# Kernel tuning notes

Measured on AMD Instinct MI355X. Metric: run time of the kernel, lower is better.

The kernel has to match this reference:

```python
import jax, jax.numpy as jnp
import numpy as np

N = 50000
E = 800000
IN_DIM = 256
HID = 256
OUT_DIM = 2


def setup_inputs() -> dict:
    key = jax.random.key(0)
    ks = jax.random.split(key, 10)
    x = jax.random.normal(ks[0], (N, IN_DIM), dtype=jnp.float32)
    edge_index = jax.random.randint(ks[1], (2, E), 0, N, dtype=jnp.int64)
    # Glorot-ish scaling so activations stay well-conditioned through 4 layers
    def w(k, fan_in, fan_out):
        return jax.random.normal(k, (fan_in, fan_out), dtype=jnp.float32) / jnp.sqrt(jnp.float32(fan_in))
    return {
        "x": x,
        "edge_index": edge_index,
        "W0": w(ks[2], IN_DIM, HID), "b0": jnp.zeros((HID,), jnp.float32),
        "W1": w(ks[3], HID, HID),    "b1": jnp.zeros((HID,), jnp.float32),
        "W2": w(ks[4], HID, HID),    "b2": jnp.zeros((HID,), jnp.float32),
        "W3": w(ks[5], HID, OUT_DIM), "b3": jnp.zeros((OUT_DIM,), jnp.float32),
    }


def _gcn_norm(edge_index, n, dtype):
    # PyG gcn_norm with self-loops: deg over destination, norm = d^-1/2[src]*d^-1/2[dst]
    loops = jnp.arange(n, dtype=edge_index.dtype)
    src = jnp.concatenate([edge_index[0], loops])
    dst = jnp.concatenate([edge_index[1], loops])
    deg = jax.ops.segment_sum(jnp.ones_like(dst, dtype=dtype), dst, num_segments=n)
    dis = deg ** -0.5  # deg >= 1 due to self-loops
    norm = dis[src] * dis[dst]
    return src, dst, norm


def reference(x, edge_index, W0, b0, W1, b1, W2, b2, W3, b3):
    n = x.shape[0]
    src, dst, norm = _gcn_norm(edge_index, n, x.dtype)

    def conv(h, W, b):
        h = h @ W                              # [N, F_out] dense GEMM
        msg = h[src] * norm[:, None]           # edge-gather + scale
        agg = jax.ops.segment_sum(msg, dst, num_segments=n)  # scatter-add
        return agg + b

    h = jax.nn.relu(conv(x, W0, b0))
    h = jax.nn.relu(conv(h, W1, b1))
    h = jax.nn.relu(conv(h, W2, b2))
    return conv(h, W3, b3)
```

## Files before the change

kernel.cpp:

```cpp
#include <hip/hip_runtime.h>

#define N_NODES 50000
#define N_EDGES 800000

static inline int cdiv(int a, int b) { return (a + b - 1) / b; }

typedef __attribute__((ext_vector_type(8))) short bf16x8;
typedef __attribute__((ext_vector_type(4))) float f32x4;
typedef __attribute__((ext_vector_type(2))) float f32x2;
typedef __attribute__((ext_vector_type(4))) unsigned int u32x4;

static __device__ __forceinline__ unsigned short f2bf(float f) {
    unsigned int u = __float_as_uint(f);
    unsigned int r = (u + 0x7FFF + ((u >> 16) & 1)) >> 16;
    return (unsigned short)r;
}
static __device__ __forceinline__ float bf2f(unsigned short h) {
    return __uint_as_float((unsigned int)h << 16);
}
static __device__ __forceinline__ float bf_lo(unsigned int u) { return __uint_as_float(u << 16); }
static __device__ __forceinline__ float bf_hi(unsigned int u) { return __uint_as_float(u & 0xFFFF0000u); }

static __device__ __forceinline__ int logc(int p) {
    int pl = p & 63;
    return (p & ~63) + (pl & 3) * 16 + (pl >> 2);
}

static __device__ __forceinline__ int2 ldnt2(const int2* p) {
    unsigned long long u = __builtin_nontemporal_load((const unsigned long long*)p);
    int2 r;
    r.x = (int)(u & 0xFFFFFFFFull);
    r.y = (int)(u >> 32);
    return r;
}

static __device__ __forceinline__ void acc8p(f32x2* acc, uint4 v, float wgt) {
    f32x2 w2;
    w2.x = wgt;
    w2.y = wgt;
    f32x2 p;
    p.x = bf_lo(v.x); p.y = bf_hi(v.x); acc[0] += p * w2;
    p.x = bf_lo(v.y); p.y = bf_hi(v.y); acc[1] += p * w2;
    p.x = bf_lo(v.z); p.y = bf_hi(v.z); acc[2] += p * w2;
    p.x = bf_lo(v.w); p.y = bf_hi(v.w); acc[3] += p * w2;
}


__global__ void k_count(const int* __restrict__ edst, int* cnt, int e) {
    int i = (blockIdx.x * 256 + threadIdx.x) * 4;
    if (i + 3 < e) {
        int4 v = *(const int4*)(edst + i);
        atomicAdd(&cnt[v.x], 1);
        atomicAdd(&cnt[v.y], 1);
        atomicAdd(&cnt[v.z], 1);
        atomicAdd(&cnt[v.w], 1);
    } else {
        for (int k = i; k < e; ++k) atomicAdd(&cnt[edst[k]], 1);
    }
}

__global__ __launch_bounds__(256) void k_scan1(const int* __restrict__ cnt,
                                               int* __restrict__ row_ptr,
                                               float* __restrict__ dis,
                                               int* __restrict__ blk, int n) {
    __shared__ int sums[256];
    int t = threadIdx.x;
    int base = blockIdx.x * 1024 + t * 4;
    int c0 = 0, c1 = 0, c2 = 0, c3 = 0;
    if (base + 3 < n) {
        int4 v = *(const int4*)(cnt + base);
        c0 = v.x + 1; c1 = v.y + 1; c2 = v.z + 1; c3 = v.w + 1;
    } else {
        if (base + 0 < n) c0 = cnt[base + 0] + 1;
        if (base + 1 < n) c1 = cnt[base + 1] + 1;
        if (base + 2 < n) c2 = cnt[base + 2] + 1;
        if (base + 3 < n) c3 = cnt[base + 3] + 1;
    }
    int s = c0 + c1 + c2 + c3;
    sums[t] = s;
    __syncthreads();
    int x = s;
    for (int off = 1; off < 256; off <<= 1) {
        int y = (t >= off) ? sums[t - off] : 0;
        __syncthreads();
        x += y;
        sums[t] = x;
        __syncthreads();
    }
    int excl = x - s;
    if (base + 0 < n) { row_ptr[base + 0] = excl;                dis[base + 0] = rsqrtf((float)c0); }
    if (base + 1 < n) { row_ptr[base + 1] = excl + c0;           dis[base + 1] = rsqrtf((float)c1); }
    if (base + 2 < n) { row_ptr[base + 2] = excl + c0 + c1;      dis[base + 2] = rsqrtf((float)c2); }
    if (base + 3 < n) { row_ptr[base + 3] = excl + c0 + c1 + c2; dis[base + 3] = rsqrtf((float)c3); }
    if (t == 255) blk[blockIdx.x] = x;
}

__global__ __launch_bounds__(256) void k_scan2(int* __restrict__ blk,
                                               int* __restrict__ row_ptr_n, int nb) {
    __shared__ int sums[256];
    int t = threadIdx.x;
    int s = (t < nb) ? blk[t] : 0;
    sums[t] = s;
    __syncthreads();
    int x = s;
    for (int off = 1; off < 256; off <<= 1) {
        int y = (t >= off) ? sums[t - off] : 0;
        __syncthreads();
        x += y;
        sums[t] = x;
        __syncthreads();
    }
    if (t < nb) blk[t] = x - s;
    if (t == 255) row_ptr_n[0] = x;
}

__global__ __launch_bounds__(256) void k_scan3(int* __restrict__ row_ptr,
                                               int* __restrict__ pos,
                                               const int* __restrict__ blk, int n) {
    int base = blockIdx.x * 1024 + threadIdx.x * 4;
    int off = blk[blockIdx.x];
#pragma unroll
    for (int i = 0; i < 4; ++i) {
        int idx = base + i;
        if (idx < n) {
            int v = row_ptr[idx] + off;
            row_ptr[idx] = v;
            pos[idx] = v;
        }
    }
}

__global__ void k_fill(const int* __restrict__ esrc, const int* __restrict__ edst,
                       int* pos, const float* __restrict__ dis,
                       int2* __restrict__ eg, int e, int n) {
    int i = blockIdx.x * 256 + threadIdx.x;
    if (i < e) {
        int s = esrc[i], d = edst[i];
        int p = atomicAdd(&pos[d], 1);
        unsigned long long u = (unsigned long long)(unsigned int)s |
                               ((unsigned long long)(unsigned int)__float_as_int(dis[s] * dis[d]) << 32);
        __builtin_nontemporal_store(u, (unsigned long long*)&eg[p]);
    } else if (i < e + n) {
        int v = i - e;
        int p = atomicAdd(&pos[v], 1);
        float dv = dis[v];
        unsigned long long u = (unsigned long long)(unsigned int)v |
                               ((unsigned long long)(unsigned int)__float_as_int(dv * dv) << 32);
        __builtin_nontemporal_store(u, (unsigned long long*)&eg[p]);
    }
}


__global__ __launch_bounds__(256) void k_prep(const float* __restrict__ W0,
                                              const float* __restrict__ W1,
                                              const float* __restrict__ W2,
                                              const float* __restrict__ b0,
                                              const float* __restrict__ b1,
                                              const float* __restrict__ b2,
                                              const float* __restrict__ W3,
                                              unsigned short* __restrict__ Wth,
                                              unsigned short* __restrict__ Wtl,
                                              float* __restrict__ bpw,
                                              const float* __restrict__ X,
                                              unsigned short* __restrict__ Xh, long total4) {
    if (blockIdx.x < 768) {
        int layer = blockIdx.x >> 8;
        int n = blockIdx.x & 255;
        int p = threadIdx.x;
        const float* W = layer == 0 ? W0 : (layer == 1 ? W1 : W2);
        int k = (layer != 0) ? logc(p) : p;
        float v = W[(size_t)k * 256 + n];
        unsigned short h = f2bf(v);
        size_t o = (size_t)layer * 65536 + (size_t)n * 256 + p;
        Wth[o] = h;
        Wtl[o] = f2bf(v - bf2f(h));
    } else if (blockIdx.x == 768) {
        int p = threadIdx.x;
        int c = logc(p);
        bpw[p] = b0[c];
        bpw[256 + p] = b1[c];
        bpw[512 + p] = b2[c];
        bpw[768 + p * 2 + 0] = W3[(size_t)c * 2 + 0];
        bpw[768 + p * 2 + 1] = W3[(size_t)c * 2 + 1];
    } else {
        long i = (long)(blockIdx.x - 769) * 256 + threadIdx.x;
        if (i >= total4) return;
        float4 v = *(const float4*)(X + i * 4);
        ushort4 h;
        h.x = f2bf(v.x);
        h.y = f2bf(v.y);
        h.z = f2bf(v.z);
        h.w = f2bf(v.w);
        *(ushort4*)(Xh + i * 4) = h;
    }
}


#define GEMM_RB 196

__global__ __launch_bounds__(256, 4) void k_gemm_mfma(const unsigned short* __restrict__ Ah,
                                                      const unsigned short* __restrict__ Wth,
                                                      const unsigned short* __restrict__ Wtl,
                                                      unsigned short* __restrict__ C, int M) {
    __shared__ unsigned short Wh[64][264];
    int rowblk = blockIdx.x % GEMM_RB;
    int colblk = blockIdx.x / GEMM_RB;
    int c0 = colblk * 64;
    int m0 = rowblk * 256;
    int t = threadIdx.x;
    int sr = t >> 2;

    {
        int hk0 = (t & 3) * 64;
        const unsigned short* gh = Wth + (size_t)(c0 + sr) * 256 + hk0;
        unsigned short* lh = &Wh[sr][hk0];
#pragma unroll
        for (int i = 0; i < 8; ++i)
            *(uint4*)(lh + i * 8) = *(const uint4*)(gh + i * 8);
    }
    __syncthreads();

    int lane = t & 63, wave = t >> 6;
    int quad = lane >> 4, l16 = lane & 15;

    const unsigned short* aph[4];
#pragma unroll
    for (int mt = 0; mt < 4; ++mt) {
        int m = m0 + wave * 64 + mt * 16 + l16;
        if (m >= M) m = M - 1;
        aph[mt] = Ah + (size_t)m * 256 + quad * 8;
    }
    const unsigned short* blp = Wtl + (size_t)(c0 + l16) * 256 + quad * 8;

    f32x4 acc[4][4];
#pragma unroll
    for (int i = 0; i < 4; ++i)
#pragma unroll
        for (int j = 0; j < 4; ++j) acc[i][j] = (f32x4){0.f, 0.f, 0.f, 0.f};

#pragma unroll 2
    for (int kc = 0; kc < 8; ++kc) {
        int ko = kc * 32;
        bf16x8 ahf[4];
#pragma unroll
        for (int mt = 0; mt < 4; ++mt) ahf[mt] = *(const bf16x8*)(aph[mt] + ko);
#pragma unroll
        for (int nt = 0; nt < 4; ++nt) {
            bf16x8 bh = *(const bf16x8*)&Wh[nt * 16 + l16][ko + quad * 8];
            bf16x8 bl = *(const bf16x8*)(blp + nt * 16 * 256 + ko);
#pragma unroll
            for (int mt = 0; mt < 4; ++mt) {
                acc[mt][nt] = __builtin_amdgcn_mfma_f32_16x16x32_bf16(ahf[mt], bh, acc[mt][nt], 0, 0, 0);
                acc[mt][nt] = __builtin_amdgcn_mfma_f32_16x16x32_bf16(ahf[mt], bl, acc[mt][nt], 0, 0, 0);
            }
        }
    }

#pragma unroll
    for (int mt = 0; mt < 4; ++mt) {
#pragma unroll
        for (int r = 0; r < 4; ++r) {
            int row = m0 + wave * 64 + mt * 16 + quad * 4 + r;
            if (row < M) {
                ushort4 sv;
                sv.x = f2bf(acc[mt][0][r]);
                sv.y = f2bf(acc[mt][1][r]);
                sv.z = f2bf(acc[mt][2][r]);
                sv.w = f2bf(acc[mt][3][r]);
                *(ushort4*)(C + (size_t)row * 256 + c0 + l16 * 4) = sv;
            }
        }
    }
}


template <int MODE>
__global__ __launch_bounds__(256, 8) void k_agg256(const unsigned short* __restrict__ t,
                                                   const int* __restrict__ row_ptr,
                                                   const int2* __restrict__ eg,
                                                   const float* __restrict__ bp,
                                                   unsigned short* __restrict__ outh,
                                                   const float* __restrict__ w3p,
                                                   float* __restrict__ t2, int n) {
    int lane = threadIdx.x & 63;
    int wave = threadIdx.x >> 6;
    int node = blockIdx.x * 4 + wave;
    if (node >= n) return;
    int half = lane >> 5;
    int fl = lane & 31;
    int beg = row_ptr[node], end = row_ptr[node + 1];
    f32x2 acc2[4];
#pragma unroll
    for (int i = 0; i < 4; ++i) { acc2[i].x = 0.f; acc2[i].y = 0.f; }
    const unsigned short* tp = t + fl * 8;

    int e = beg + half;
    for (; e + 10 < end; e += 12) {
        int2 a0 = ldnt2(eg + e), a1 = ldnt2(eg + e + 2), a2 = ldnt2(eg + e + 4);
        int2 a3 = ldnt2(eg + e + 6), a4 = ldnt2(eg + e + 8), a5 = ldnt2(eg + e + 10);
        uint4 v0 = *(const uint4*)(tp + (size_t)a0.x * 256);
        uint4 v1 = *(const uint4*)(tp + (size_t)a1.x * 256);
        uint4 v2 = *(const uint4*)(tp + (size_t)a2.x * 256);
        uint4 v3 = *(const uint4*)(tp + (size_t)a3.x * 256);
        uint4 v4 = *(const uint4*)(tp + (size_t)a4.x * 256);
        uint4 v5 = *(const uint4*)(tp + (size_t)a5.x * 256);
        acc8p(acc2, v0, __int_as_float(a0.y));
        acc8p(acc2, v1, __int_as_float(a1.y));
        acc8p(acc2, v2, __int_as_float(a2.y));
        acc8p(acc2, v3, __int_as_float(a3.y));
        acc8p(acc2, v4, __int_as_float(a4.y));
        acc8p(acc2, v5, __int_as_float(a5.y));
    }
    for (; e + 6 < end; e += 8) {
        int2 a0 = ldnt2(eg + e), a1 = ldnt2(eg + e + 2);
        int2 a2 = ldnt2(eg + e + 4), a3 = ldnt2(eg + e + 6);
        uint4 v0 = *(const uint4*)(tp + (size_t)a0.x * 256);
        uint4 v1 = *(const uint4*)(tp + (size_t)a1.x * 256);
        uint4 v2 = *(const uint4*)(tp + (size_t)a2.x * 256);
        uint4 v3 = *(const uint4*)(tp + (size_t)a3.x * 256);
        acc8p(acc2, v0, __int_as_float(a0.y));
        acc8p(acc2, v1, __int_as_float(a1.y));
        acc8p(acc2, v2, __int_as_float(a2.y));
        acc8p(acc2, v3, __int_as_float(a3.y));
    }
    for (; e + 2 < end; e += 4) {
        int2 a0 = ldnt2(eg + e), a1 = ldnt2(eg + e + 2);
        uint4 v0 = *(const uint4*)(tp + (size_t)a0.x * 256);
        uint4 v1 = *(const uint4*)(tp + (size_t)a1.x * 256);
        acc8p(acc2, v0, __int_as_float(a0.y));
        acc8p(acc2, v1, __int_as_float(a1.y));
    }
    if (e < end) {
        int2 a0 = ldnt2(eg + e);
        uint4 v0 = *(const uint4*)(tp + (size_t)a0.x * 256);
        acc8p(acc2, v0, __int_as_float(a0.y));
    }

    float va[8];
#pragma unroll
    for (int i = 0; i < 4; ++i) { va[2 * i] = acc2[i].x; va[2 * i + 1] = acc2[i].y; }
#pragma unroll
    for (int i = 0; i < 8; ++i) va[i] += __shfl_xor(va[i], 32);

    if (MODE == 0) {
        if (half == 0) {
            float4 bA = *(const float4*)(bp + fl * 8);
            float4 bB = *(const float4*)(bp + fl * 8 + 4);
            float r0 = fmaxf(va[0] + bA.x, 0.f), r1 = fmaxf(va[1] + bA.y, 0.f);
            float r2 = fmaxf(va[2] + bA.z, 0.f), r3 = fmaxf(va[3] + bA.w, 0.f);
            float r4 = fmaxf(va[4] + bB.x, 0.f), r5 = fmaxf(va[5] + bB.y, 0.f);
            float r6 = fmaxf(va[6] + bB.z, 0.f), r7 = fmaxf(va[7] + bB.w, 0.f);
            u32x4 w;
            w.x = (unsigned)f2bf(r0) | ((unsigned)f2bf(r1) << 16);
            w.y = (unsigned)f2bf(r2) | ((unsigned)f2bf(r3) << 16);
            w.z = (unsigned)f2bf(r4) | ((unsigned)f2bf(r5) << 16);
            w.w = (unsigned)f2bf(r6) | ((unsigned)f2bf(r7) << 16);
            __builtin_nontemporal_store(w, (u32x4*)(outh + (size_t)node * 256 + fl * 8));
        }
    } else {
        float4 bA = *(const float4*)(bp + fl * 8);
        float4 bB = *(const float4*)(bp + fl * 8 + 4);
        float r0 = fmaxf(va[0] + bA.x, 0.f), r1 = fmaxf(va[1] + bA.y, 0.f);
        float r2 = fmaxf(va[2] + bA.z, 0.f), r3 = fmaxf(va[3] + bA.w, 0.f);
        float r4 = fmaxf(va[4] + bB.x, 0.f), r5 = fmaxf(va[5] + bB.y, 0.f);
        float r6 = fmaxf(va[6] + bB.z, 0.f), r7 = fmaxf(va[7] + bB.w, 0.f);
        const float* wp = w3p + fl * 16;
        float4 wA = *(const float4*)(wp + 0);
        float4 wB = *(const float4*)(wp + 4);
        float4 wC = *(const float4*)(wp + 8);
        float4 wD = *(const float4*)(wp + 12);
        float s0 = r0 * wA.x + r1 * wA.z + r2 * wB.x + r3 * wB.z +
                   r4 * wC.x + r5 * wC.z + r6 * wD.x + r7 * wD.z;
        float s1 = r0 * wA.y + r1 * wA.w + r2 * wB.y + r3 * wB.w +
                   r4 * wC.y + r5 * wC.w + r6 * wD.y + r7 * wD.w;
#pragma unroll
        for (int off = 16; off > 0; off >>= 1) {
            s0 += __shfl_xor(s0, off);
            s1 += __shfl_xor(s1, off);
        }
        if (lane == 0) {
            f32x2 o;
            o.x = s0;
            o.y = s1;
            __builtin_nontemporal_store(o, (f32x2*)(t2 + (size_t)node * 2));
        }
    }
}


__global__ void k_agg2(const float* __restrict__ t2,
                       const int* __restrict__ row_ptr,
                       const int2* __restrict__ eg,
                       const float* __restrict__ b3,
                       float* __restrict__ out, int n) {
    int tid = blockIdx.x * 256 + threadIdx.x;
    int node = tid >> 2;
    int sub = tid & 3;
    if (node >= n) return;
    int beg = row_ptr[node], end = row_ptr[node + 1];
    float a0 = 0.f, a1 = 0.f;
    for (int e = beg + sub; e < end; e += 4) {
        int2 m = ldnt2(eg + e);
        float w = __int_as_float(m.y);
        float2 v = *(const float2*)(t2 + (size_t)m.x * 2);
        a0 += w * v.x;
        a1 += w * v.y;
    }
    a0 += __shfl_xor(a0, 1); a1 += __shfl_xor(a1, 1);
    a0 += __shfl_xor(a0, 2); a1 += __shfl_xor(a1, 2);
    if (sub == 0) {
        out[(size_t)node * 2 + 0] = a0 + b3[0];
        out[(size_t)node * 2 + 1] = a1 + b3[1];
    }
}


extern "C" void kernel_launch(void* const* d_in, const int* in_sizes, int n_in,
                              void* d_out, int out_size, void* d_ws, size_t ws_size,
                              hipStream_t stream) {
    const int N = N_NODES, E = N_EDGES;
    const float* x  = (const float*)d_in[0];
    const int* ei   = (const int*)d_in[1];
    const int* esrc = ei;
    const int* edst = ei + E;
    const float* W0 = (const float*)d_in[2];
    const float* b0 = (const float*)d_in[3];
    const float* W1 = (const float*)d_in[4];
    const float* b1 = (const float*)d_in[5];
    const float* W2 = (const float*)d_in[6];
    const float* b2 = (const float*)d_in[7];
    const float* W3 = (const float*)d_in[8];
    const float* b3 = (const float*)d_in[9];
    float* out = (float*)d_out;

    unsigned short* Ahh = (unsigned short*)d_ws;
    unsigned short* Tb  = Ahh + (size_t)N * 256;
    unsigned short* Wth = Tb + (size_t)N * 256;
    unsigned short* Wtl = Wth + 3 * 65536;
    int2*  eg     = (int2*)(Wtl + 3 * 65536);
    float* t2     = (float*)(eg + (E + N));
    float* bpw    = t2 + (size_t)N * 2;
    float* dis    = bpw + 1280;
    int*   cnt    = (int*)(dis + N);
    int*   row_ptr= cnt + N;
    int*   pos    = row_ptr + (N + 1);
    int*   blk    = pos + N;

    const int NB = cdiv(N, 1024);

    hipMemsetAsync(cnt, 0, (size_t)N * sizeof(int), stream);
    k_count<<<cdiv(E, 1024), 256, 0, stream>>>(edst, cnt, E);
    k_scan1<<<NB, 256, 0, stream>>>(cnt, row_ptr, dis, blk, N);
    k_scan2<<<1, 256, 0, stream>>>(blk, row_ptr + N, NB);
    k_scan3<<<NB, 256, 0, stream>>>(row_ptr, pos, blk, N);
    k_fill<<<cdiv(E + N, 256), 256, 0, stream>>>(esrc, edst, pos, dis, eg, E, N);

    const int ggrid = GEMM_RB * 4;
    const int agrid = cdiv(N, 4);
    const long total4 = (long)N * 64;
    const int CA = cdiv((int)total4, 256);

    k_prep<<<769 + CA, 256, 0, stream>>>(W0, W1, W2, b0, b1, b2, W3, Wth, Wtl, bpw, x, Ahh, total4);

    k_gemm_mfma<<<ggrid, 256, 0, stream>>>(Ahh, Wth, Wtl, Tb, N);
    k_agg256<0><<<agrid, 256, 0, stream>>>(Tb, row_ptr, eg, bpw, Ahh, nullptr, nullptr, N);
    k_gemm_mfma<<<ggrid, 256, 0, stream>>>(Ahh, Wth + 65536, Wtl + 65536, Tb, N);
    k_agg256<0><<<agrid, 256, 0, stream>>>(Tb, row_ptr, eg, bpw + 256, Ahh, nullptr, nullptr, N);
    k_gemm_mfma<<<ggrid, 256, 0, stream>>>(Ahh, Wth + 2 * 65536, Wtl + 2 * 65536, Tb, N);
    k_agg256<1><<<agrid, 256, 0, stream>>>(Tb, row_ptr, eg, bpw + 512, nullptr, bpw + 768, t2, N);
    k_agg2<<<cdiv(4 * N, 256), 256, 0, stream>>>(t2, row_ptr, eg, b3, out, N);
}
```

Measured before the change: 498.4 us.

## Tile weight transpose through LDS and remap GEMM block order for XCD locality

```diff
diff --git a/kernel.cpp b/kernel.cpp
--- a/kernel.cpp
+++ b/kernel.cpp
@@ -20,11 +20,6 @@
 }
 static __device__ __forceinline__ float bf_lo(unsigned int u) { return __uint_as_float(u << 16); }
 static __device__ __forceinline__ float bf_hi(unsigned int u) { return __uint_as_float(u & 0xFFFF0000u); }
-
-static __device__ __forceinline__ int logc(int p) {
-    int pl = p & 63;
-    return (p & ~63) + (pl & 3) * 16 + (pl >> 2);
-}
 
 static __device__ __forceinline__ int2 ldnt2(const int2* p) {
     unsigned long long u = __builtin_nontemporal_load((const unsigned long long*)p);
@@ -163,27 +158,47 @@
                                               float* __restrict__ bpw,
                                               const float* __restrict__ X,
                                               unsigned short* __restrict__ Xh, long total4) {
-    if (blockIdx.x < 768) {
-        int layer = blockIdx.x >> 8;
-        int n = blockIdx.x & 255;
+    if (blockIdx.x < 48) {
+        __shared__ float tile[64][65];
+        int layer = blockIdx.x / 16;
+        int tid = blockIdx.x % 16;
+        int ti = tid >> 2, tj = tid & 3;
+        const float* W = layer == 0 ? W0 : (layer == 1 ? W1 : W2);
+        int r0 = ti * 64, n0 = tj * 64;
+        int rr = threadIdx.x >> 4;
+        int cc = (threadIdx.x & 15) * 4;
+#pragma unroll
+        for (int j = 0; j < 4; ++j) {
+            float4 v = *(const float4*)(W + (size_t)(r0 + rr + j * 16) * 256 + n0 + cc);
+            tile[rr + j * 16][cc + 0] = v.x;
+            tile[rr + j * 16][cc + 1] = v.y;
+            tile[rr + j * 16][cc + 2] = v.z;
+            tile[rr + j * 16][cc + 3] = v.w;
+        }
+        __syncthreads();
+        int pl = threadIdx.x & 63;
+        int ng = threadIdx.x >> 6;
+        int kl = (layer != 0) ? ((pl & 3) * 16 + (pl >> 2)) : pl;
+#pragma unroll
+        for (int i = 0; i < 16; ++i) {
+            int nl = ng * 16 + i;
+            float v = tile[kl][nl];
+            unsigned short h = f2bf(v);
+            size_t o = (size_t)layer * 65536 + (size_t)(n0 + nl) * 256 + r0 + pl;
+            Wth[o] = h;
+            Wtl[o] = f2bf(v - bf2f(h));
+        }
+    } else if (blockIdx.x == 48) {
         int p = threadIdx.x;
-        const float* W = layer == 0 ? W0 : (layer == 1 ? W1 : W2);
-        int k = (layer != 0) ? logc(p) : p;
-        float v = W[(size_t)k * 256 + n];
-        unsigned short h = f2bf(v);
-        size_t o = (size_t)layer * 65536 + (size_t)n * 256 + p;
-        Wth[o] = h;
-        Wtl[o] = f2bf(v - bf2f(h));
-    } else if (blockIdx.x == 768) {
-        int p = threadIdx.x;
-        int c = logc(p);
+        int pl = p & 63;
+        int c = (p & ~63) + (pl & 3) * 16 + (pl >> 2);
         bpw[p] = b0[c];
         bpw[256 + p] = b1[c];
         bpw[512 + p] = b2[c];
         bpw[768 + p * 2 + 0] = W3[(size_t)c * 2 + 0];
         bpw[768 + p * 2 + 1] = W3[(size_t)c * 2 + 1];
     } else {
-        long i = (long)(blockIdx.x - 769) * 256 + threadIdx.x;
+        long i = (long)(blockIdx.x - 49) * 256 + threadIdx.x;
         if (i >= total4) return;
         float4 v = *(const float4*)(X + i * 4);
         ushort4 h;
@@ -197,15 +212,19 @@
 
 
 #define GEMM_RB 196
+#define GEMM_GRID (((GEMM_RB + 7) / 8) * 32)
 
 __global__ __launch_bounds__(256, 4) void k_gemm_mfma(const unsigned short* __restrict__ Ah,
                                                       const unsigned short* __restrict__ Wth,
                                                       const unsigned short* __restrict__ Wtl,
                                                       unsigned short* __restrict__ C, int M) {
     __shared__ unsigned short Wh[64][264];
-    int rowblk = blockIdx.x % GEMM_RB;
-    int colblk = blockIdx.x / GEMM_RB;
-    int c0 = colblk * 64;
+    int x = blockIdx.x & 7;
+    int t5 = blockIdx.x >> 3;
+    int q = t5 >> 2, cb = t5 & 3;
+    int rowblk = q * 8 + x;
+    if (rowblk >= GEMM_RB) return;
+    int c0 = cb * 64;
     int m0 = rowblk * 256;
     int t = threadIdx.x;
     int sr = t >> 2;
@@ -455,18 +474,17 @@
     k_scan3<<<NB, 256, 0, stream>>>(row_ptr, pos, blk, N);
     k_fill<<<cdiv(E + N, 256), 256, 0, stream>>>(esrc, edst, pos, dis, eg, E, N);
 
-    const int ggrid = GEMM_RB * 4;
     const int agrid = cdiv(N, 4);
     const long total4 = (long)N * 64;
     const int CA = cdiv((int)total4, 256);
 
-    k_prep<<<769 + CA, 256, 0, stream>>>(W0, W1, W2, b0, b1, b2, W3, Wth, Wtl, bpw, x, Ahh, total4);
-
-    k_gemm_mfma<<<ggrid, 256, 0, stream>>>(Ahh, Wth, Wtl, Tb, N);
+    k_prep<<<49 + CA, 256, 0, stream>>>(W0, W1, W2, b0, b1, b2, W3, Wth, Wtl, bpw, x, Ahh, total4);
+
+    k_gemm_mfma<<<GEMM_GRID, 256, 0, stream>>>(Ahh, Wth, Wtl, Tb, N);
     k_agg256<0><<<agrid, 256, 0, stream>>>(Tb, row_ptr, eg, bpw, Ahh, nullptr, nullptr, N);
-    k_gemm_mfma<<<ggrid, 256, 0, stream>>>(Ahh, Wth + 65536, Wtl + 65536, Tb, N);
+    k_gemm_mfma<<<GEMM_GRID, 256, 0, stream>>>(Ahh, Wth + 65536, Wtl + 65536, Tb, N);
     k_agg256<0><<<agrid, 256, 0, stream>>>(Tb, row_ptr, eg, bpw + 256, Ahh, nullptr, nullptr, N);
-    k_gemm_mfma<<<ggrid, 256, 0, stream>>>(Ahh, Wth + 2 * 65536, Wtl + 2 * 65536, Tb, N);
+    k_gemm_mfma<<<GEMM_GRID, 256, 0, stream>>>(Ahh, Wth + 2 * 65536, Wtl + 2 * 65536, Tb, N);
     k_agg256<1><<<agrid, 256, 0, stream>>>(Tb, row_ptr, eg, bpw + 512, nullptr, bpw + 768, t2, N);
     k_agg2<<<cdiv(4 * N, 256), 256, 0, stream>>>(t2, row_ptr, eg, b3, out, N);
 }
```

New measurement: 503.8 us. Within noise of the previous version (+1.1%).
